# Kernel optimization log

Measured on AMD Instinct MI355X. Metric: run time of the kernel, lower is better.

Reference implementation:

```python
import jax, jax.numpy as jnp
import numpy as np

NUM_HEADS = 12
HEAD_DIM = 64
LOGIT_SCALE_MAX = 4.605170185988092  # log(1/0.01), open_clip default
EPS = 1e-12  # F.normalize eps


def setup_inputs() -> dict:
    key = jax.random.key(0)
    ks = jax.random.split(key, 8)
    N, L, C = 2, 2048, 768
    return {
        "x": jax.random.normal(ks[0], (N, L, C), dtype=jnp.float32),
        "in_proj_w": jax.random.normal(ks[1], (3 * C, C), dtype=jnp.float32) * 0.02,
        "in_proj_b": jax.random.normal(ks[2], (3 * C,), dtype=jnp.float32) * 0.02,
        "logit_scale": jax.random.normal(ks[3], (NUM_HEADS, 1, 1), dtype=jnp.float32),
        "learned_scale": jnp.ones((NUM_HEADS,), dtype=jnp.float32),
        "out_proj_w": jax.random.normal(ks[4], (C, C), dtype=jnp.float32) * 0.02,
        "out_proj_b": jax.random.normal(ks[5], (C,), dtype=jnp.float32) * 0.02,
        "attn_mask": jnp.zeros((L, L), dtype=jnp.float32),
    }


def _l2norm(t):
    # F.normalize(dim=-1): x / max(||x||, eps)
    n = jnp.linalg.norm(t, axis=-1, keepdims=True)
    return t / jnp.maximum(n, EPS)


def reference(x, in_proj_w, in_proj_b, logit_scale, learned_scale,
              out_proj_w, out_proj_b, attn_mask):
    N, L, C = x.shape
    H, D = NUM_HEADS, HEAD_DIM
    # packed QKV projection: [N, L, 3C]
    qkv = jnp.einsum("nlc,fc->nlf", x, in_proj_w) + in_proj_b
    q, k, v = jnp.split(qkv, 3, axis=-1)
    # [N, L, C] -> [N, H, L, D]
    to_heads = lambda t: t.reshape(N, L, H, D).transpose(0, 2, 1, 3)
    q, k, v = to_heads(q), to_heads(k), to_heads(v)
    # cosine attention with clamped exp logit scale per head
    attn = jnp.einsum("nhld,nhmd->nhlm", _l2norm(q), _l2norm(k))
    ls = jnp.exp(jnp.minimum(logit_scale, LOGIT_SCALE_MAX))  # [H,1,1]
    attn = attn * ls[None]  # broadcast over [N,H,L,L]
    attn = attn + attn_mask  # additive mask [L,L]
    attn = jax.nn.softmax(attn, axis=-1)
    out = jnp.einsum("nhlm,nhmd->nhld", attn, v)
    # learned per-head output scale
    out = out * learned_scale[None, :, None, None]
    # [N,H,L,D] -> [N,L,C]
    out = out.transpose(0, 2, 1, 3).reshape(N, L, C)
    out = jnp.einsum("nlc,fc->nlf", out, out_proj_w) + out_proj_b
    return out
```

## Files before the change

### kernel.cpp

```cpp
#include <hip/hip_runtime.h>
#include <math.h>

#define NB   2
#define SEQ  2048
#define CH   768
#define NH   12
#define HD   64
#define F3   2304
#define LSMAX 4.605170185988092f
#define LOG2E 1.4426950408889634f

typedef _Float16 f16;
typedef __attribute__((ext_vector_type(8))) _Float16 f16x8;
typedef __attribute__((ext_vector_type(4))) _Float16 f16x4;
typedef __attribute__((ext_vector_type(2))) _Float16 f16x2;
typedef __attribute__((ext_vector_type(4))) float f32x4;

#define QSZ   3145728
#define OATT  (3 * QSZ)
#define XHOFF 12582912
#define W1OFF 15728640
#define W2OFF 17498112
#define MOFF  18087936
#define FLAGO 22282240

#define PIT  72
#define PPIT 76
#define GP   40

__global__ __launch_bounds__(256) void cvt_f16(const float* __restrict__ X,
                                               const float* __restrict__ W1,
                                               const float* __restrict__ W2,
                                               const float* __restrict__ M,
                                               f16* __restrict__ Xh,
                                               f16* __restrict__ W1h,
                                               f16* __restrict__ W2h,
                                               f16* __restrict__ Mh,
                                               int* __restrict__ flag)
{
    int tid = blockIdx.x * 256 + threadIdx.x;
    const float* src; f16* dst; int n4;
    switch (blockIdx.y) {
        case 0:  src = X;  dst = Xh;  n4 = 786432;  break;
        case 1:  src = W1; dst = W1h; n4 = 442368;  break;
        case 2:  src = W2; dst = W2h; n4 = 147456;  break;
        default: src = M;  dst = Mh;  n4 = 1048576; break;
    }
    if (tid < n4) {
        float4 v = ((const float4*)src)[tid];
        if (blockIdx.y == 3) {
            bool nz = (v.x != 0.f) || (v.y != 0.f) || (v.z != 0.f) || (v.w != 0.f);
            if (__any(nz) && (threadIdx.x & 63) == 0) atomicOr(flag, 1);
            v.x *= LOG2E; v.y *= LOG2E; v.z *= LOG2E; v.w *= LOG2E;
        }
        f16x4 o = {(f16)v.x, (f16)v.y, (f16)v.z, (f16)v.w};
        ((f16x4*)dst)[tid] = o;
    }
}

__global__ __launch_bounds__(256, 3) void qkv_gemm(const f16* __restrict__ Xh,
                                                   const f16* __restrict__ Wh,
                                                   const float* __restrict__ bias,
                                                   const float* __restrict__ logit_scale,
                                                   f16* __restrict__ qkv16)
{
    __shared__ f16 As[128 * GP];
    __shared__ f16 Bs[128 * GP];
    const int t    = threadIdx.x;
    const int w    = t >> 6;
    const int lane = t & 63;
    const int quad = lane >> 4;
    const int sub  = lane & 15;
    const int wm   = w & 1, wn = w >> 1;
    const int f0   = blockIdx.x * 128;
    const int m0   = blockIdx.y * 128;
    const int srow = t >> 1;
    const int sk   = (t & 1) * 16;

    const f16* ag = Xh + (size_t)(m0 + srow) * CH + sk;
    const f16* bg = Wh + (size_t)(f0 + srow) * CH + sk;
    f16x8 a0 = *(const f16x8*)(ag);
    f16x8 a1 = *(const f16x8*)(ag + 8);
    f16x8 b0 = *(const f16x8*)(bg);
    f16x8 b1 = *(const f16x8*)(bg + 8);

    f32x4 acc[4][4];
#pragma unroll
    for (int i = 0; i < 4; ++i)
#pragma unroll
        for (int j = 0; j < 4; ++j) acc[i][j] = (f32x4){0.f, 0.f, 0.f, 0.f};

    for (int k0 = 0; k0 < CH; k0 += 32) {
        __syncthreads();
        *(f16x8*)&As[srow * GP + sk + 0] = a0;
        *(f16x8*)&As[srow * GP + sk + 8] = a1;
        *(f16x8*)&Bs[srow * GP + sk + 0] = b0;
        *(f16x8*)&Bs[srow * GP + sk + 8] = b1;
        __syncthreads();
        if (k0 + 32 < CH) {
            a0 = *(const f16x8*)(ag + k0 + 32);
            a1 = *(const f16x8*)(ag + k0 + 40);
            b0 = *(const f16x8*)(bg + k0 + 32);
            b1 = *(const f16x8*)(bg + k0 + 40);
        }
        f16x8 af[4], bf[4];
#pragma unroll
        for (int i = 0; i < 4; ++i) {
            af[i] = *(const f16x8*)&As[(wm * 64 + i * 16 + sub) * GP + quad * 8];
            bf[i] = *(const f16x8*)&Bs[(wn * 64 + i * 16 + sub) * GP + quad * 8];
        }
#pragma unroll
        for (int i = 0; i < 4; ++i)
#pragma unroll
            for (int j = 0; j < 4; ++j)
                acc[i][j] = __builtin_amdgcn_mfma_f32_16x16x32_f16(af[i], bf[j], acc[i][j], 0, 0, 0);
    }

    const int t3 = f0 / CH;
    const int h  = ((f0 + wn * 64) % CH) >> 6;
    f16* dst = qkv16 + (size_t)t3 * QSZ;
    float lsv = (t3 == 0) ? __expf(fminf(logit_scale[h], LSMAX)) * LOG2E : 1.0f;
    float bb[4];
#pragma unroll
    for (int j = 0; j < 4; ++j) bb[j] = bias[f0 + wn * 64 + j * 16 + sub];
#pragma unroll
    for (int i = 0; i < 4; ++i) {
#pragma unroll
        for (int r = 0; r < 4; ++r) {
            int m = m0 + wm * 64 + i * 16 + quad * 4 + r;
            int n = m >> 11, l = m & 2047;
            float v[4];
#pragma unroll
            for (int j = 0; j < 4; ++j) v[j] = acc[i][j][r] + bb[j];
            float scale = 1.0f;
            if (t3 < 2) {
                float ss = v[0] * v[0] + v[1] * v[1] + v[2] * v[2] + v[3] * v[3];
#pragma unroll
                for (int mk = 1; mk < 16; mk <<= 1) ss += __shfl_xor(ss, mk, 64);
                scale = 1.0f / fmaxf(sqrtf(ss), 1e-12f);
                if (t3 == 0) scale *= lsv;
            }
            f16* drow = dst + (((size_t)n * NH + h) * SEQ + l) * HD;
#pragma unroll
            for (int j = 0; j < 4; ++j)
                drow[j * 16 + sub] = (f16)(v[j] * scale);
        }
    }
}

__global__ __launch_bounds__(256, 3) void attn(const f16* __restrict__ Qh,
                                               const f16* __restrict__ Kh,
                                               const f16* __restrict__ Vh,
                                               const f16* __restrict__ Mh,
                                               const float* __restrict__ lscale,
                                               const int* __restrict__ flag,
                                               f16* __restrict__ Og)
{
    __shared__ f16 Ks[2][64 * PIT];
    __shared__ f16 Vt[2][64 * PIT];
    __shared__ f16 QP[64 * PPIT];

    const int t    = threadIdx.x;
    const int w    = t >> 6;
    const int lane = t & 63;
    const int quad = lane >> 4;
    const int sub  = lane & 15;
    const int qb   = blockIdx.x * 64;
    const int h    = blockIdx.y, n = blockIdx.z;
    const bool has_mask = (*flag) != 0;

    const f16* Qg = Qh + ((size_t)(n * NH + h) * SEQ + qb) * HD;
    const f16* Kg = Kh + (size_t)(n * NH + h) * SEQ * HD;
    const f16* Vg = Vh + (size_t)(n * NH + h) * SEQ * HD;
    const f16* Mg = Mh + (size_t)(qb + w * 16 + quad * 4) * SEQ;

#pragma unroll
    for (int rep = 0; rep < 2; ++rep) {
        int id = rep * 256 + t;
        int row = id >> 3, c8 = id & 7;
        f16x8 v = *(const f16x8*)&Qg[row * 64 + c8 * 8];
        *(f16x4*)&QP[row * PPIT + c8 * 8 + 0] = (f16x4){v[0], v[1], v[2], v[3]};
        *(f16x4*)&QP[row * PPIT + c8 * 8 + 4] = (f16x4){v[4], v[5], v[6], v[7]};
    }

    const int krow = t >> 3, kc8 = t & 7;
    f16x8 kr0 = *(const f16x8*)&Kg[krow * 64 + kc8 * 8];
    f16x8 kr1 = *(const f16x8*)&Kg[(32 + krow) * 64 + kc8 * 8];
    f16x8 vr0 = *(const f16x8*)&Vg[lane * 64 + w * 16];
    f16x8 vr1 = *(const f16x8*)&Vg[lane * 64 + w * 16 + 8];
    f16 mnxt[16];
    if (has_mask) {
#pragma unroll
        for (int ct = 0; ct < 4; ++ct)
#pragma unroll
            for (int r = 0; r < 4; ++r)
                mnxt[ct * 4 + r] = Mg[(size_t)r * SEQ + ct * 16 + sub];
    }

    __syncthreads();
    f16x8 qf0, qf1;
    {
        f16x4 l0 = *(const f16x4*)&QP[(w * 16 + sub) * PPIT + quad * 8];
        f16x4 l1 = *(const f16x4*)&QP[(w * 16 + sub) * PPIT + quad * 8 + 4];
        f16x4 l2 = *(const f16x4*)&QP[(w * 16 + sub) * PPIT + 32 + quad * 8];
        f16x4 l3 = *(const f16x4*)&QP[(w * 16 + sub) * PPIT + 32 + quad * 8 + 4];
        qf0 = (f16x8){l0[0], l0[1], l0[2], l0[3], l1[0], l1[1], l1[2], l1[3]};
        qf1 = (f16x8){l2[0], l2[1], l2[2], l2[3], l3[0], l3[1], l3[2], l3[3]};
    }

    *(f16x8*)&Ks[0][krow * PIT + kc8 * 8] = kr0;
    *(f16x8*)&Ks[0][(32 + krow) * PIT + kc8 * 8] = kr1;
#pragma unroll
    for (int j = 0; j < 8; ++j) {
        Vt[0][(w * 16 + j) * PIT + lane] = vr0[j];
        Vt[0][(w * 16 + 8 + j) * PIT + lane] = vr1[j];
    }
    {
        const f16* Kn = Kg + 64 * 64;
        const f16* Vn = Vg + 64 * 64;
        kr0 = *(const f16x8*)&Kn[krow * 64 + kc8 * 8];
        kr1 = *(const f16x8*)&Kn[(32 + krow) * 64 + kc8 * 8];
        vr0 = *(const f16x8*)&Vn[lane * 64 + w * 16];
        vr1 = *(const f16x8*)&Vn[lane * 64 + w * 16 + 8];
    }

    const f16x8 ones = {(f16)1.f, (f16)1.f, (f16)1.f, (f16)1.f,
                        (f16)1.f, (f16)1.f, (f16)1.f, (f16)1.f};
    f32x4 o[4];
    f32x4 l_acc = (f32x4){0.f, 0.f, 0.f, 0.f};
    float m_run[4];
#pragma unroll
    for (int dt = 0; dt < 4; ++dt) o[dt] = (f32x4){0.f, 0.f, 0.f, 0.f};
#pragma unroll
    for (int r = 0; r < 4; ++r) m_run[r] = -1e30f;

    const int NC = SEQ / 64;
    for (int c = 0; c < NC; ++c) {
        __syncthreads();
        const int cur = c & 1, nxt = cur ^ 1;
        if (c + 1 < NC) {
            *(f16x8*)&Ks[nxt][krow * PIT + kc8 * 8] = kr0;
            *(f16x8*)&Ks[nxt][(32 + krow) * PIT + kc8 * 8] = kr1;
#pragma unroll
            for (int j = 0; j < 8; ++j) {
                Vt[nxt][(w * 16 + j) * PIT + lane] = vr0[j];
                Vt[nxt][(w * 16 + 8 + j) * PIT + lane] = vr1[j];
            }
            if (c + 2 < NC) {
                const f16* Kn = Kg + (c + 2) * 64 * 64;
                const f16* Vn = Vg + (c + 2) * 64 * 64;
                kr0 = *(const f16x8*)&Kn[krow * 64 + kc8 * 8];
                kr1 = *(const f16x8*)&Kn[(32 + krow) * 64 + kc8 * 8];
                vr0 = *(const f16x8*)&Vn[lane * 64 + w * 16];
                vr1 = *(const f16x8*)&Vn[lane * 64 + w * 16 + 8];
            }
        }
        f16 mcur[16];
        if (has_mask) {
#pragma unroll
            for (int i = 0; i < 16; ++i) mcur[i] = mnxt[i];
            if (c + 1 < NC) {
#pragma unroll
                for (int ct = 0; ct < 4; ++ct)
#pragma unroll
                    for (int r = 0; r < 4; ++r)
                        mnxt[ct * 4 + r] = Mg[(size_t)r * SEQ + (c + 1) * 64 + ct * 16 + sub];
            }
        }

        f32x4 s[4];
#pragma unroll
        for (int ct = 0; ct < 4; ++ct) {
            f16x8 kf0 = *(const f16x8*)&Ks[cur][(ct * 16 + sub) * PIT + quad * 8];
            f16x8 kf1 = *(const f16x8*)&Ks[cur][(ct * 16 + sub) * PIT + 32 + quad * 8];
            f32x4 a = (f32x4){0.f, 0.f, 0.f, 0.f};
            a = __builtin_amdgcn_mfma_f32_16x16x32_f16(qf0, kf0, a, 0, 0, 0);
            a = __builtin_amdgcn_mfma_f32_16x16x32_f16(qf1, kf1, a, 0, 0, 0);
            s[ct] = a;
        }
        if (has_mask) {
#pragma unroll
            for (int ct = 0; ct < 4; ++ct)
#pragma unroll
                for (int r = 0; r < 4; ++r)
                    s[ct][r] += (float)mcur[ct * 4 + r];
        }
        float mnew[4];
#pragma unroll
        for (int r = 0; r < 4; ++r)
            mnew[r] = fmaxf(fmaxf(fmaxf(s[0][r], s[1][r]), fmaxf(s[2][r], s[3][r])), m_run[r]);
        {
            union { f16x2 h; int i; } p0, p1, v0, v1;
            p0.h = (f16x2){(f16)mnew[0], (f16)mnew[1]};
            p1.h = (f16x2){(f16)mnew[2], (f16)mnew[3]};
#pragma unroll
            for (int mk = 1; mk < 16; mk <<= 1) {
                v0.i = __shfl_xor(p0.i, mk, 64);
                v1.i = __shfl_xor(p1.i, mk, 64);
                p0.h = __builtin_elementwise_max(p0.h, v0.h);
                p1.h = __builtin_elementwise_max(p1.h, v1.h);
            }
            mnew[0] = (float)p0.h[0]; mnew[1] = (float)p0.h[1];
            mnew[2] = (float)p1.h[0]; mnew[3] = (float)p1.h[1];
        }
        float alpha[4];
#pragma unroll
        for (int r = 0; r < 4; ++r) {
            alpha[r] = exp2f(m_run[r] - mnew[r]);
            m_run[r] = mnew[r];
        }
#pragma unroll
        for (int ct = 0; ct < 4; ++ct)
#pragma unroll
            for (int r = 0; r < 4; ++r) {
                float p = exp2f(s[ct][r] - mnew[r]);
                QP[(w * 16 + quad * 4 + r) * PPIT + ct * 16 + sub] = (f16)p;
            }
#pragma unroll
        for (int dt = 0; dt < 4; ++dt)
#pragma unroll
            for (int r = 0; r < 4; ++r) o[dt][r] *= alpha[r];
#pragma unroll
        for (int r = 0; r < 4; ++r) l_acc[r] *= alpha[r];
        f16x4 p00 = *(const f16x4*)&QP[(w * 16 + sub) * PPIT + quad * 8];
        f16x4 p01 = *(const f16x4*)&QP[(w * 16 + sub) * PPIT + quad * 8 + 4];
        f16x4 p10 = *(const f16x4*)&QP[(w * 16 + sub) * PPIT + 32 + quad * 8];
        f16x4 p11 = *(const f16x4*)&QP[(w * 16 + sub) * PPIT + 32 + quad * 8 + 4];
        f16x8 pf0 = {p00[0], p00[1], p00[2], p00[3], p01[0], p01[1], p01[2], p01[3]};
        f16x8 pf1 = {p10[0], p10[1], p10[2], p10[3], p11[0], p11[1], p11[2], p11[3]};
        l_acc = __builtin_amdgcn_mfma_f32_16x16x32_f16(pf0, ones, l_acc, 0, 0, 0);
        l_acc = __builtin_amdgcn_mfma_f32_16x16x32_f16(pf1, ones, l_acc, 0, 0, 0);
#pragma unroll
        for (int dt = 0; dt < 4; ++dt) {
            f16x8 vf0 = *(const f16x8*)&Vt[cur][(dt * 16 + sub) * PIT + quad * 8];
            f16x8 vf1 = *(const f16x8*)&Vt[cur][(dt * 16 + sub) * PIT + 32 + quad * 8];
            o[dt] = __builtin_amdgcn_mfma_f32_16x16x32_f16(pf0, vf0, o[dt], 0, 0, 0);
            o[dt] = __builtin_amdgcn_mfma_f32_16x16x32_f16(pf1, vf1, o[dt], 0, 0, 0);
        }
    }
    float lsc = lscale[h];
#pragma unroll
    for (int r = 0; r < 4; ++r) {
        float inv = lsc / l_acc[r];
        int q = qb + w * 16 + quad * 4 + r;
#pragma unroll
        for (int dt = 0; dt < 4; ++dt)
            Og[((size_t)n * SEQ + q) * CH + h * 64 + dt * 16 + sub] =
                (f16)(o[dt][r] * inv);
    }
}

__global__ __launch_bounds__(256, 3) void out_gemm(const f16* __restrict__ A,
                                                   const f16* __restrict__ Wh,
                                                   const float* __restrict__ bias,
                                                   float* __restrict__ out)
{
    __shared__ f16 As[128 * GP];
    __shared__ f16 Bs[128 * GP];
    const int t    = threadIdx.x;
    const int w    = t >> 6;
    const int lane = t & 63;
    const int quad = lane >> 4;
    const int sub  = lane & 15;
    const int wm   = w & 1, wn = w >> 1;
    const int f0   = blockIdx.x * 128;
    const int m0   = blockIdx.y * 128;
    const int srow = t >> 1;
    const int sk   = (t & 1) * 16;

    const f16* ag = A + (size_t)(m0 + srow) * CH + sk;
    const f16* bg = Wh + (size_t)(f0 + srow) * CH + sk;
    f16x8 a0 = *(const f16x8*)(ag);
    f16x8 a1 = *(const f16x8*)(ag + 8);
    f16x8 b0 = *(const f16x8*)(bg);
    f16x8 b1 = *(const f16x8*)(bg + 8);

    f32x4 acc[4][4];
#pragma unroll
    for (int i = 0; i < 4; ++i)
#pragma unroll
        for (int j = 0; j < 4; ++j) acc[i][j] = (f32x4){0.f, 0.f, 0.f, 0.f};

    for (int k0 = 0; k0 < CH; k0 += 32) {
        __syncthreads();
        *(f16x8*)&As[srow * GP + sk + 0] = a0;
        *(f16x8*)&As[srow * GP + sk + 8] = a1;
        *(f16x8*)&Bs[srow * GP + sk + 0] = b0;
        *(f16x8*)&Bs[srow * GP + sk + 8] = b1;
        __syncthreads();
        if (k0 + 32 < CH) {
            a0 = *(const f16x8*)(ag + k0 + 32);
            a1 = *(const f16x8*)(ag + k0 + 40);
            b0 = *(const f16x8*)(bg + k0 + 32);
            b1 = *(const f16x8*)(bg + k0 + 40);
        }
        f16x8 af[4], bf[4];
#pragma unroll
        for (int i = 0; i < 4; ++i) {
            af[i] = *(const f16x8*)&As[(wm * 64 + i * 16 + sub) * GP + quad * 8];
            bf[i] = *(const f16x8*)&Bs[(wn * 64 + i * 16 + sub) * GP + quad * 8];
        }
#pragma unroll
        for (int i = 0; i < 4; ++i)
#pragma unroll
            for (int j = 0; j < 4; ++j)
                acc[i][j] = __builtin_amdgcn_mfma_f32_16x16x32_f16(af[i], bf[j], acc[i][j], 0, 0, 0);
    }
    float bb[4];
#pragma unroll
    for (int j = 0; j < 4; ++j) bb[j] = bias[f0 + wn * 64 + j * 16 + sub];
#pragma unroll
    for (int i = 0; i < 4; ++i)
#pragma unroll
        for (int r = 0; r < 4; ++r) {
            int m = m0 + wm * 64 + i * 16 + quad * 4 + r;
            float* orow = out + (size_t)m * CH + f0 + wn * 64;
#pragma unroll
            for (int j = 0; j < 4; ++j)
                orow[j * 16 + sub] = acc[i][j][r] + bb[j];
        }
}

extern "C" void kernel_launch(void* const* d_in, const int* in_sizes, int n_in,
                              void* d_out, int out_size, void* d_ws, size_t ws_size,
                              hipStream_t stream) {
    const float* x    = (const float*)d_in[0];
    const float* w1   = (const float*)d_in[1];
    const float* b1   = (const float*)d_in[2];
    const float* ls   = (const float*)d_in[3];
    const float* lrn  = (const float*)d_in[4];
    const float* w2   = (const float*)d_in[5];
    const float* b2   = (const float*)d_in[6];
    const float* msk  = (const float*)d_in[7];
    f16*   ws16 = (f16*)d_ws;
    int*   flag = (int*)(ws16 + FLAGO);
    float* out  = (float*)d_out;

    (void)hipMemsetAsync(flag, 0, 4, stream);
    hipLaunchKernelGGL(cvt_f16, dim3(4096, 4), dim3(256), 0, stream,
                       x, w1, w2, msk,
                       ws16 + XHOFF, ws16 + W1OFF, ws16 + W2OFF, ws16 + MOFF, flag);
    hipLaunchKernelGGL(qkv_gemm, dim3(F3 / 128, (NB * SEQ) / 128), dim3(256), 0, stream,
                       ws16 + XHOFF, ws16 + W1OFF, b1, ls, ws16);
    hipLaunchKernelGGL(attn, dim3(SEQ / 64, NH, NB), dim3(256), 0, stream,
                       ws16, ws16 + QSZ, ws16 + 2 * QSZ, ws16 + MOFF, lrn, flag,
                       ws16 + OATT);
    hipLaunchKernelGGL(out_gemm, dim3(CH / 128, (NB * SEQ) / 128), dim3(256), 0, stream,
                       ws16 + OATT, ws16 + W2OFF, b2, out);
}
```

Baseline: 227.5 us.

## Process 128-key tiles per attention iteration and stop converting the mask to fp16

The attention loop now stages 128 keys per iteration in a single shared buffer with a register prefetch, instead of double-buffered 64-key tiles. This halves the number of loop iterations and softmax max/rescale steps, at the cost of two barriers per iteration and no LDS double buffering. The conversion kernel now only scans the mask for nonzeros and no longer writes an fp16 copy, which removes a large store. When the mask is nonzero, attn reads the fp32 mask directly and applies LOG2E itself.

Result: faster. 212.0 us (-6.8%).

```diff
diff --git a/kernel.cpp b/kernel.cpp
--- a/kernel.cpp
+++ b/kernel.cpp
@@ -21,10 +21,10 @@
 #define XHOFF 12582912
 #define W1OFF 15728640
 #define W2OFF 17498112
-#define MOFF  18087936
-#define FLAGO 22282240
-
-#define PIT  72
+#define FLAGO 18087936
+
+#define KP   72
+#define VP   136
 #define PPIT 76
 #define GP   40
 
@@ -35,24 +35,25 @@
                                                f16* __restrict__ Xh,
                                                f16* __restrict__ W1h,
                                                f16* __restrict__ W2h,
-                                               f16* __restrict__ Mh,
                                                int* __restrict__ flag)
 {
     int tid = blockIdx.x * 256 + threadIdx.x;
+    if (blockIdx.y == 3) {
+        if (tid < 1048576) {
+            float4 v = ((const float4*)M)[tid];
+            bool nz = (v.x != 0.f) || (v.y != 0.f) || (v.z != 0.f) || (v.w != 0.f);
+            if (__any(nz) && (threadIdx.x & 63) == 0) atomicOr(flag, 1);
+        }
+        return;
+    }
     const float* src; f16* dst; int n4;
     switch (blockIdx.y) {
         case 0:  src = X;  dst = Xh;  n4 = 786432;  break;
         case 1:  src = W1; dst = W1h; n4 = 442368;  break;
-        case 2:  src = W2; dst = W2h; n4 = 147456;  break;
-        default: src = M;  dst = Mh;  n4 = 1048576; break;
+        default: src = W2; dst = W2h; n4 = 147456;  break;
     }
     if (tid < n4) {
         float4 v = ((const float4*)src)[tid];
-        if (blockIdx.y == 3) {
-            bool nz = (v.x != 0.f) || (v.y != 0.f) || (v.z != 0.f) || (v.w != 0.f);
-            if (__any(nz) && (threadIdx.x & 63) == 0) atomicOr(flag, 1);
-            v.x *= LOG2E; v.y *= LOG2E; v.z *= LOG2E; v.w *= LOG2E;
-        }
         f16x4 o = {(f16)v.x, (f16)v.y, (f16)v.z, (f16)v.w};
         ((f16x4*)dst)[tid] = o;
     }
@@ -151,13 +152,13 @@
 __global__ __launch_bounds__(256, 3) void attn(const f16* __restrict__ Qh,
                                                const f16* __restrict__ Kh,
                                                const f16* __restrict__ Vh,
-                                               const f16* __restrict__ Mh,
+                                               const float* __restrict__ M32,
                                                const float* __restrict__ lscale,
                                                const int* __restrict__ flag,
                                                f16* __restrict__ Og)
 {
-    __shared__ f16 Ks[2][64 * PIT];
-    __shared__ f16 Vt[2][64 * PIT];
+    __shared__ f16 Ks[128 * KP];
+    __shared__ f16 Vt[64 * VP];
     __shared__ f16 QP[64 * PPIT];
 
     const int t    = threadIdx.x;
@@ -172,7 +173,7 @@
     const f16* Qg = Qh + ((size_t)(n * NH + h) * SEQ + qb) * HD;
     const f16* Kg = Kh + (size_t)(n * NH + h) * SEQ * HD;
     const f16* Vg = Vh + (size_t)(n * NH + h) * SEQ * HD;
-    const f16* Mg = Mh + (size_t)(qb + w * 16 + quad * 4) * SEQ;
+    const float* Mg = M32 + (size_t)(qb + w * 16 + quad * 4) * SEQ;
 
 #pragma unroll
     for (int rep = 0; rep < 2; ++rep) {
@@ -183,18 +184,20 @@
         *(f16x4*)&QP[row * PPIT + c8 * 8 + 4] = (f16x4){v[4], v[5], v[6], v[7]};
     }
 
-    const int krow = t >> 3, kc8 = t & 7;
-    f16x8 kr0 = *(const f16x8*)&Kg[krow * 64 + kc8 * 8];
-    f16x8 kr1 = *(const f16x8*)&Kg[(32 + krow) * 64 + kc8 * 8];
-    f16x8 vr0 = *(const f16x8*)&Vg[lane * 64 + w * 16];
-    f16x8 vr1 = *(const f16x8*)&Vg[lane * 64 + w * 16 + 8];
-    f16 mnxt[16];
-    if (has_mask) {
-#pragma unroll
-        for (int ct = 0; ct < 4; ++ct)
-#pragma unroll
-            for (int r = 0; r < 4; ++r)
-                mnxt[ct * 4 + r] = Mg[(size_t)r * SEQ + ct * 16 + sub];
+    const int krow = t >> 1;
+    const int kcb  = (t & 1) * 32;
+    f16x8 kr0, kr1, kr2, kr3, vr0, vr1, vr2, vr3;
+    {
+        const f16* kp = Kg + krow * 64 + kcb;
+        kr0 = *(const f16x8*)(kp + 0);
+        kr1 = *(const f16x8*)(kp + 8);
+        kr2 = *(const f16x8*)(kp + 16);
+        kr3 = *(const f16x8*)(kp + 24);
+        const f16* vp = Vg + (2 * lane) * 64 + w * 16;
+        vr0 = *(const f16x8*)(vp + 0);
+        vr1 = *(const f16x8*)(vp + 8);
+        vr2 = *(const f16x8*)(vp + 64);
+        vr3 = *(const f16x8*)(vp + 72);
     }
 
     __syncthreads();
@@ -208,21 +211,19 @@
         qf1 = (f16x8){l2[0], l2[1], l2[2], l2[3], l3[0], l3[1], l3[2], l3[3]};
     }
 
-    *(f16x8*)&Ks[0][krow * PIT + kc8 * 8] = kr0;
-    *(f16x8*)&Ks[0][(32 + krow) * PIT + kc8 * 8] = kr1;
-#pragma unroll
-    for (int j = 0; j < 8; ++j) {
-        Vt[0][(w * 16 + j) * PIT + lane] = vr0[j];
-        Vt[0][(w * 16 + 8 + j) * PIT + lane] = vr1[j];
-    }
     {
-        const f16* Kn = Kg + 64 * 64;
-        const f16* Vn = Vg + 64 * 64;
-        kr0 = *(const f16x8*)&Kn[krow * 64 + kc8 * 8];
-        kr1 = *(const f16x8*)&Kn[(32 + krow) * 64 + kc8 * 8];
-        vr0 = *(const f16x8*)&Vn[lane * 64 + w * 16];
-        vr1 = *(const f16x8*)&Vn[lane * 64 + w * 16 + 8];
-    }
+        f16* kd = &Ks[krow * KP + kcb];
+        *(f16x8*)(kd + 0)  = kr0;
+        *(f16x8*)(kd + 8)  = kr1;
+        *(f16x8*)(kd + 16) = kr2;
+        *(f16x8*)(kd + 24) = kr3;
+#pragma unroll
+        for (int j = 0; j < 8; ++j) {
+            *(f16x2*)&Vt[(w * 16 + j) * VP + 2 * lane]     = (f16x2){vr0[j], vr2[j]};
+            *(f16x2*)&Vt[(w * 16 + 8 + j) * VP + 2 * lane] = (f16x2){vr1[j], vr3[j]};
+        }
+    }
+    __syncthreads();
 
     const f16x8 ones = {(f16)1.f, (f16)1.f, (f16)1.f, (f16)1.f,
                         (f16)1.f, (f16)1.f, (f16)1.f, (f16)1.f};
@@ -234,45 +235,27 @@
 #pragma unroll
     for (int r = 0; r < 4; ++r) m_run[r] = -1e30f;
 
-    const int NC = SEQ / 64;
-    for (int c = 0; c < NC; ++c) {
-        __syncthreads();
-        const int cur = c & 1, nxt = cur ^ 1;
-        if (c + 1 < NC) {
-            *(f16x8*)&Ks[nxt][krow * PIT + kc8 * 8] = kr0;
-            *(f16x8*)&Ks[nxt][(32 + krow) * PIT + kc8 * 8] = kr1;
-#pragma unroll
-            for (int j = 0; j < 8; ++j) {
-                Vt[nxt][(w * 16 + j) * PIT + lane] = vr0[j];
-                Vt[nxt][(w * 16 + 8 + j) * PIT + lane] = vr1[j];
-            }
-            if (c + 2 < NC) {
-                const f16* Kn = Kg + (c + 2) * 64 * 64;
-                const f16* Vn = Vg + (c + 2) * 64 * 64;
-                kr0 = *(const f16x8*)&Kn[krow * 64 + kc8 * 8];
-                kr1 = *(const f16x8*)&Kn[(32 + krow) * 64 + kc8 * 8];
-                vr0 = *(const f16x8*)&Vn[lane * 64 + w * 16];
-                vr1 = *(const f16x8*)&Vn[lane * 64 + w * 16 + 8];
-            }
-        }
-        f16 mcur[16];
-        if (has_mask) {
-#pragma unroll
-            for (int i = 0; i < 16; ++i) mcur[i] = mnxt[i];
-            if (c + 1 < NC) {
-#pragma unroll
-                for (int ct = 0; ct < 4; ++ct)
-#pragma unroll
-                    for (int r = 0; r < 4; ++r)
-                        mnxt[ct * 4 + r] = Mg[(size_t)r * SEQ + (c + 1) * 64 + ct * 16 + sub];
-            }
-        }
-
-        f32x4 s[4];
-#pragma unroll
-        for (int ct = 0; ct < 4; ++ct) {
-            f16x8 kf0 = *(const f16x8*)&Ks[cur][(ct * 16 + sub) * PIT + quad * 8];
-            f16x8 kf1 = *(const f16x8*)&Ks[cur][(ct * 16 + sub) * PIT + 32 + quad * 8];
+    const int NITER = SEQ / 128;
+    for (int c = 0; c < NITER; ++c) {
+        const int c0 = c * 128;
+        if (c + 1 < NITER) {
+            const f16* kp = Kg + (c0 + 128 + krow) * 64 + kcb;
+            kr0 = *(const f16x8*)(kp + 0);
+            kr1 = *(const f16x8*)(kp + 8);
+            kr2 = *(const f16x8*)(kp + 16);
+            kr3 = *(const f16x8*)(kp + 24);
+            const f16* vp = Vg + (c0 + 128 + 2 * lane) * 64 + w * 16;
+            vr0 = *(const f16x8*)(vp + 0);
+            vr1 = *(const f16x8*)(vp + 8);
+            vr2 = *(const f16x8*)(vp + 64);
+            vr3 = *(const f16x8*)(vp + 72);
+        }
+
+        f32x4 s[8];
+#pragma unroll
+        for (int ct = 0; ct < 8; ++ct) {
+            f16x8 kf0 = *(const f16x8*)&Ks[(ct * 16 + sub) * KP + quad * 8];
+            f16x8 kf1 = *(const f16x8*)&Ks[(ct * 16 + sub) * KP + 32 + quad * 8];
             f32x4 a = (f32x4){0.f, 0.f, 0.f, 0.f};
             a = __builtin_amdgcn_mfma_f32_16x16x32_f16(qf0, kf0, a, 0, 0, 0);
             a = __builtin_amdgcn_mfma_f32_16x16x32_f16(qf1, kf1, a, 0, 0, 0);
@@ -280,15 +263,18 @@
         }
         if (has_mask) {
 #pragma unroll
-            for (int ct = 0; ct < 4; ++ct)
+            for (int ct = 0; ct < 8; ++ct)
 #pragma unroll
                 for (int r = 0; r < 4; ++r)
-                    s[ct][r] += (float)mcur[ct * 4 + r];
+                    s[ct][r] += LOG2E * Mg[(size_t)r * SEQ + c0 + ct * 16 + sub];
         }
         float mnew[4];
 #pragma unroll
-        for (int r = 0; r < 4; ++r)
-            mnew[r] = fmaxf(fmaxf(fmaxf(s[0][r], s[1][r]), fmaxf(s[2][r], s[3][r])), m_run[r]);
+        for (int r = 0; r < 4; ++r) {
+            float a01 = fmaxf(s[0][r], s[1][r]), a23 = fmaxf(s[2][r], s[3][r]);
+            float a45 = fmaxf(s[4][r], s[5][r]), a67 = fmaxf(s[6][r], s[7][r]);
+            mnew[r] = fmaxf(fmaxf(fmaxf(a01, a23), fmaxf(a45, a67)), m_run[r]);
+        }
         {
             union { f16x2 h; int i; } p0, p1, v0, v1;
             p0.h = (f16x2){(f16)mnew[0], (f16)mnew[1]};
@@ -310,32 +296,51 @@
             m_run[r] = mnew[r];
         }
 #pragma unroll
-        for (int ct = 0; ct < 4; ++ct)
-#pragma unroll
-            for (int r = 0; r < 4; ++r) {
-                float p = exp2f(s[ct][r] - mnew[r]);
-                QP[(w * 16 + quad * 4 + r) * PPIT + ct * 16 + sub] = (f16)p;
+        for (int dt = 0; dt < 4; ++dt)
+#pragma unroll
+            for (int r = 0; r < 4; ++r) o[dt][r] *= alpha[r];
+#pragma unroll
+        for (int r = 0; r < 4; ++r) l_acc[r] *= alpha[r];
+
+#pragma unroll
+        for (int hf = 0; hf < 2; ++hf) {
+#pragma unroll
+            for (int ct = 0; ct < 4; ++ct)
+#pragma unroll
+                for (int r = 0; r < 4; ++r) {
+                    float p = exp2f(s[hf * 4 + ct][r] - mnew[r]);
+                    QP[(w * 16 + quad * 4 + r) * PPIT + ct * 16 + sub] = (f16)p;
+                }
+            f16x4 p00 = *(const f16x4*)&QP[(w * 16 + sub) * PPIT + quad * 8];
+            f16x4 p01 = *(const f16x4*)&QP[(w * 16 + sub) * PPIT + quad * 8 + 4];
+            f16x4 p10 = *(const f16x4*)&QP[(w * 16 + sub) * PPIT + 32 + quad * 8];
+            f16x4 p11 = *(const f16x4*)&QP[(w * 16 + sub) * PPIT + 32 + quad * 8 + 4];
+            f16x8 pf0 = {p00[0], p00[1], p00[2], p00[3], p01[0], p01[1], p01[2], p01[3]};
+            f16x8 pf1 = {p10[0], p10[1], p10[2], p10[3], p11[0], p11[1], p11[2], p11[3]};
+            l_acc = __builtin_amdgcn_mfma_f32_16x16x32_f16(pf0, ones, l_acc, 0, 0, 0);
+            l_acc = __builtin_amdgcn_mfma_f32_16x16x32_f16(pf1, ones, l_acc, 0, 0, 0);
+#pragma unroll
+            for (int dt = 0; dt < 4; ++dt) {
+                f16x8 vf0 = *(const f16x8*)&Vt[(dt * 16 + sub) * VP + hf * 64 + quad * 8];
+                f16x8 vf1 = *(const f16x8*)&Vt[(dt * 16 + sub) * VP + hf * 64 + 32 + quad * 8];
+                o[dt] = __builtin_amdgcn_mfma_f32_16x16x32_f16(pf0, vf0, o[dt], 0, 0, 0);
+                o[dt] = __builtin_amdgcn_mfma_f32_16x16x32_f16(pf1, vf1, o[dt], 0, 0, 0);
             }
-#pragma unroll
-        for (int dt = 0; dt < 4; ++dt)
-#pragma unroll
-            for (int r = 0; r < 4; ++r) o[dt][r] *= alpha[r];
-#pragma unroll
-        for (int r = 0; r < 4; ++r) l_acc[r] *= alpha[r];
-        f16x4 p00 = *(const f16x4*)&QP[(w * 16 + sub) * PPIT + quad * 8];
-        f16x4 p01 = *(const f16x4*)&QP[(w * 16 + sub) * PPIT + quad * 8 + 4];
-        f16x4 p10 = *(const f16x4*)&QP[(w * 16 + sub) * PPIT + 32 + quad * 8];
-        f16x4 p11 = *(const f16x4*)&QP[(w * 16 + sub) * PPIT + 32 + quad * 8 + 4];
-        f16x8 pf0 = {p00[0], p00[1], p00[2], p00[3], p01[0], p01[1], p01[2], p01[3]};
-        f16x8 pf1 = {p10[0], p10[1], p10[2], p10[3], p11[0], p11[1], p11[2], p11[3]};
-        l_acc = __builtin_amdgcn_mfma_f32_16x16x32_f16(pf0, ones, l_acc, 0, 0, 0);
-        l_acc = __builtin_amdgcn_mfma_f32_16x16x32_f16(pf1, ones, l_acc, 0, 0, 0);
-#pragma unroll
-        for (int dt = 0; dt < 4; ++dt) {
-            f16x8 vf0 = *(const f16x8*)&Vt[cur][(dt * 16 + sub) * PIT + quad * 8];
-            f16x8 vf1 = *(const f16x8*)&Vt[cur][(dt * 16 + sub) * PIT + 32 + quad * 8];
-            o[dt] = __builtin_amdgcn_mfma_f32_16x16x32_f16(pf0, vf0, o[dt], 0, 0, 0);
-            o[dt] = __builtin_amdgcn_mfma_f32_16x16x32_f16(pf1, vf1, o[dt], 0, 0, 0);
+        }
+
+        if (c + 1 < NITER) {
+            __syncthreads();
+            f16* kd = &Ks[krow * KP + kcb];
+            *(f16x8*)(kd + 0)  = kr0;
+            *(f16x8*)(kd + 8)  = kr1;
+            *(f16x8*)(kd + 16) = kr2;
+            *(f16x8*)(kd + 24) = kr3;
+#pragma unroll
+            for (int j = 0; j < 8; ++j) {
+                *(f16x2*)&Vt[(w * 16 + j) * VP + 2 * lane]     = (f16x2){vr0[j], vr2[j]};
+                *(f16x2*)&Vt[(w * 16 + 8 + j) * VP + 2 * lane] = (f16x2){vr1[j], vr3[j]};
+            }
+            __syncthreads();
         }
     }
     float lsc = lscale[h];
@@ -439,11 +444,11 @@
     (void)hipMemsetAsync(flag, 0, 4, stream);
     hipLaunchKernelGGL(cvt_f16, dim3(4096, 4), dim3(256), 0, stream,
                        x, w1, w2, msk,
-                       ws16 + XHOFF, ws16 + W1OFF, ws16 + W2OFF, ws16 + MOFF, flag);
+                       ws16 + XHOFF, ws16 + W1OFF, ws16 + W2OFF, flag);
     hipLaunchKernelGGL(qkv_gemm, dim3(F3 / 128, (NB * SEQ) / 128), dim3(256), 0, stream,
                        ws16 + XHOFF, ws16 + W1OFF, b1, ls, ws16);
     hipLaunchKernelGGL(attn, dim3(SEQ / 64, NH, NB), dim3(256), 0, stream,
-                       ws16, ws16 + QSZ, ws16 + 2 * QSZ, ws16 + MOFF, lrn, flag,
+                       ws16, ws16 + QSZ, ws16 + 2 * QSZ, msk, lrn, flag,
                        ws16 + OATT);
     hipLaunchKernelGGL(out_gemm, dim3(CH / 128, (NB * SEQ) / 128), dim3(256), 0, stream,
                        ws16 + OATT, ws16 + W2OFF, b2, out);
```
